# Performance work log

Measured on AMD Instinct MI355X. Metric: run time of the kernel, lower is better.

## Reference

```python
import jax, jax.numpy as jnp
import numpy as np

N = 50000      # ncount
IN_CH = 256    # in_channels
OUT_CH = 128   # out_channels
NNZ = 800000   # nnz per sparse matrix (avg degree 16)


def _spmm(rows, cols, vals, dense, n_rows):
    # sparse(COO) @ dense : gather rows of dense by col index, scale, scatter-add by row
    contrib = vals[:, None] * dense[cols]              # [nnz, F]
    return jax.ops.segment_sum(contrib, rows, num_segments=n_rows)


def setup_inputs() -> dict:
    key = jax.random.key(0)
    ks = jax.random.split(key, 12)
    phi_indices = jnp.stack([
        jax.random.randint(ks[0], (NNZ,), 0, N),
        jax.random.randint(ks[1], (NNZ,), 0, N)])
    phi_values = jax.random.normal(ks[2], (NNZ,), dtype=jnp.float32)
    phi_inverse_indices = jnp.stack([
        jax.random.randint(ks[3], (NNZ,), 0, N),
        jax.random.randint(ks[4], (NNZ,), 0, N)])
    phi_inverse_values = jax.random.normal(ks[5], (NNZ,), dtype=jnp.float32)
    feature_indices = jnp.stack([
        jax.random.randint(ks[6], (NNZ,), 0, N),       # node index
        jax.random.randint(ks[7], (NNZ,), 0, IN_CH)])  # feature column
    feature_values = jax.random.normal(ks[8], (NNZ,), dtype=jnp.float32)
    # xavier_uniform for weight_matrix
    limit = float(np.sqrt(6.0 / (IN_CH + OUT_CH)))
    weight_matrix = jax.random.uniform(ks[9], (IN_CH, OUT_CH), jnp.float32, -limit, limit)
    # diagonal filter Theta init uniform(0.9, 1.1)
    diagonal_weight_filter = jax.random.uniform(ks[10], (N,), jnp.float32, 0.9, 1.1)
    return {
        "phi_indices": phi_indices,
        "phi_values": phi_values,
        "phi_inverse_indices": phi_inverse_indices,
        "phi_inverse_values": phi_inverse_values,
        "feature_indices": feature_indices,
        "feature_values": feature_values,
        "weight_matrix": weight_matrix,
        "diagonal_weight_filter": diagonal_weight_filter,
        "dropout": 0,
    }


def reference(phi_indices, phi_values, phi_inverse_indices, phi_inverse_values,
              feature_indices, feature_values, weight_matrix,
              diagonal_weight_filter, dropout):
    # rescaled_phi = phi @ diag(theta): scales column j of phi by theta[j]
    scaled_phi_vals = phi_values * diagonal_weight_filter[phi_indices[1]]
    # filtered = features(sparse N x IN) @ W  -> [N, OUT]
    filtered = _spmm(feature_indices[0], feature_indices[1], feature_values,
                     weight_matrix, N)
    # (phi * D * phi_inv) @ filtered computed associatively without dense N x N:
    tmp = _spmm(phi_inverse_indices[0], phi_inverse_indices[1],
                phi_inverse_values, filtered, N)              # phi_inv @ filtered
    localized = _spmm(phi_indices[0], phi_indices[1],
                      scaled_phi_vals, tmp, N)                # (phi D) @ tmp
    # dropout in eval mode (training=False) is identity
    return jax.nn.relu(localized)
```

## Files before the change

### kernel.cpp

```cpp
#include <hip/hip_runtime.h>
#include <hip/hip_fp16.h>


#define OUT_CH 128
#define HALF_CH 64
#define RPB 256
#define RPB_SHIFT 8
#define MAX_NB 256
#define EPB 4096
#define EPT_C 8
#define EPT_D 16
#define STAGE_CAP 8192
#define MAX_INCH_LDS 256


__global__ __launch_bounds__(512) void bucket_hist_kernel(
    const int* __restrict__ rows0, int n0,
    const int* __restrict__ rows1, int n1,
    const int* __restrict__ rows2, int n2,
    int* __restrict__ hist_part,
    int NB, int NBLK)
{
    int m = blockIdx.y;
    const int* rows = (m == 0) ? rows0 : (m == 1) ? rows1 : rows2;
    int nnz         = (m == 0) ? n0    : (m == 1) ? n1    : n2;
    __shared__ int bins[MAX_NB];
    int t = threadIdx.x;
    if (t < NB) bins[t] = 0;
    __syncthreads();
    int base = blockIdx.x * EPB;
    #pragma unroll
    for (int k = 0; k < EPB / 512; ++k) {
        int i = base + k * 512 + t;
        if (i < nnz) atomicAdd(&bins[rows[i] >> RPB_SHIFT], 1);
    }
    __syncthreads();
    int* out = hist_part + ((size_t)(m * NBLK + blockIdx.x)) * NB;
    if (t < NB) out[t] = bins[t];
}


__global__ __launch_bounds__(256) void reduce_totals_kernel(
    const int* __restrict__ hist_part, int* __restrict__ totals, int NB, int NBLK)
{
    int w = blockIdx.x * 4 + (threadIdx.x >> 6);
    if (w >= 3 * NB) return;
    int lane = threadIdx.x & 63;
    int m = w / NB, b = w - m * NB;
    const int* hp = hist_part + (size_t)m * NBLK * NB + b;
    int sum = 0;
    for (int blk = lane; blk < NBLK; blk += 64)
        sum += hp[(size_t)blk * NB];
    #pragma unroll
    for (int s = 1; s < 64; s <<= 1) sum += __shfl_xor(sum, s);
    if (lane == 0) totals[w] = sum;
}


__global__ __launch_bounds__(256) void scan_bases_kernel(
    const int* __restrict__ totals, int* __restrict__ bases,
    int* __restrict__ cursor, int NB)
{
    int m = blockIdx.x, t = threadIdx.x;
    int x = (t < NB) ? totals[m * NB + t] : 0;
    int lane = t & 63, wid = t >> 6;
    int incl = x;
    #pragma unroll
    for (int s = 1; s < 64; s <<= 1) {
        int y = __shfl_up(incl, s);
        if (lane >= s) incl += y;
    }
    __shared__ int wtot[4], wbase[4];
    if (lane == 63) wtot[wid] = incl;
    __syncthreads();
    if (t == 0) {
        int run = 0;
        #pragma unroll
        for (int w = 0; w < 4; ++w) { int v = wtot[w]; wbase[w] = run; run += v; }
    }
    __syncthreads();
    if (t < NB) {
        int excl = wbase[wid] + incl - x;
        bases[m * NB + t] = excl;
        cursor[m * NB + t] = excl;
    }
}


__global__ __launch_bounds__(512) void bucket_scatter_kernel(
    const int* __restrict__ rows0, const int* __restrict__ cols0, const float* __restrict__ vals0, int n0,
    const int* __restrict__ rows1, const int* __restrict__ cols1, const float* __restrict__ vals1, int n1,
    const int* __restrict__ rows2, const int* __restrict__ cols2, const float* __restrict__ vals2, int n2,
    const float* __restrict__ theta,
    const int* __restrict__ hist_part, int* __restrict__ cursor,
    int2* __restrict__ eb0, int2* __restrict__ eb1, int2* __restrict__ eb2,
    int NB, int NBLK)
{
    int m = blockIdx.y;
    const int* rows; const int* cols; const float* vals; int nnz; int2* eb;
    if (m == 0)      { rows = rows0; cols = cols0; vals = vals0; nnz = n0; eb = eb0; }
    else if (m == 1) { rows = rows1; cols = cols1; vals = vals1; nnz = n1; eb = eb1; }
    else             { rows = rows2; cols = cols2; vals = vals2; nnz = n2; eb = eb2; }

    __shared__ int2 staged[EPB];
    __shared__ unsigned char bucket_of[EPB];
    __shared__ int lstart[MAX_NB];
    __shared__ int lcur[MAX_NB];
    __shared__ int gbase[MAX_NB];
    __shared__ int wtot[8], wbase[8];

    int t = threadIdx.x;
    int base = blockIdx.x * EPB;
    bool fold = (m == 2);

    int  bk[EPT_C];
    int2 pl[EPT_C];
    #pragma unroll
    for (int k = 0; k < EPT_C; ++k) {
        int i = base + k * 512 + t;
        if (i < nnz) {
            int r = rows[i], c = cols[i];
            float v = vals[i];
            if (fold) v *= theta[c];
            bk[k] = r >> RPB_SHIFT;
            pl[k] = make_int2(c | ((r & (RPB - 1)) << 16), __float_as_int(v));
        } else bk[k] = -1;
    }

    {
        const int* hp = hist_part + ((size_t)(m * NBLK + blockIdx.x)) * NB;
        int lh = (t < NB) ? hp[t] : 0;
        int lane = t & 63, wid = t >> 6;
        int incl = lh;
        #pragma unroll
        for (int s = 1; s < 64; s <<= 1) {
            int y = __shfl_up(incl, s);
            if (lane >= s) incl += y;
        }
        if (lane == 63) wtot[wid] = incl;
        __syncthreads();
        if (t == 0) {
            int run = 0;
            #pragma unroll
            for (int w = 0; w < 8; ++w) { int v = wtot[w]; wbase[w] = run; run += v; }
        }
        __syncthreads();
        if (t < NB) {
            int excl = wbase[wid] + incl - lh;
            lstart[t] = excl;
            lcur[t]   = excl;
            gbase[t] = atomicAdd(&cursor[m * NB + t], lh);
        }
    }
    __syncthreads();

    #pragma unroll
    for (int k = 0; k < EPT_C; ++k) {
        if (bk[k] >= 0) {
            int idx = atomicAdd(&lcur[bk[k]], 1);
            staged[idx] = pl[k];
            bucket_of[idx] = (unsigned char)bk[k];
        }
    }
    __syncthreads();

    int count = min(EPB, nnz - base);
    for (int i = t; i < count; i += 512) {
        int b = bucket_of[i];
        int dest = gbase[b] + (i - lstart[b]);
        eb[dest] = staged[i];
    }
}


__global__ __launch_bounds__(512) void bucket_to_csr_kernel(
    const int2* __restrict__ eb0, const int2* __restrict__ eb1, const int2* __restrict__ eb2,
    unsigned int* __restrict__ ec0, unsigned int* __restrict__ ec1, unsigned int* __restrict__ ec2,
    const int* __restrict__ bases,
    int* __restrict__ off,
    int n0, int n1, int n2, int NB, int n)
{
    int m = blockIdx.y;
    int b = blockIdx.x;
    const int2* eb; unsigned int* ec; int nnz;
    if (m == 0)      { eb = eb0; ec = ec0; nnz = n0; }
    else if (m == 1) { eb = eb1; ec = ec1; nnz = n1; }
    else             { eb = eb2; ec = ec2; nnz = n2; }
    int base = bases[m * NB + b];
    int end  = (b + 1 < NB) ? bases[m * NB + b + 1] : nnz;
    int cnt  = end - base;

    __shared__ unsigned int staged_c[STAGE_CAP];
    __shared__ int hist[RPB];
    __shared__ int cur[RPB];
    __shared__ int loc[RPB + 1];
    __shared__ int wtot[4];
    __shared__ int wbase[4];
    int t = threadIdx.x;
    int lane = t & 63, wid = t >> 6;
    if (t < RPB) { hist[t] = 0; cur[t] = 0; }
    __syncthreads();

    bool fits = (cnt <= STAGE_CAP);

    int2 er[EPT_D];
    int  rl[EPT_D];
    if (fits) {
        #pragma unroll
        for (int k = 0; k < EPT_D; ++k) {
            int i = base + k * 512 + t;
            if (i < end) {
                er[k] = eb[i];
                rl[k] = (er[k].x >> 16) & (RPB - 1);
                atomicAdd(&hist[rl[k]], 1);
            } else rl[k] = -1;
        }
    } else {
        for (int i = base + t; i < end; i += 512)
            atomicAdd(&hist[(eb[i].x >> 16) & (RPB - 1)], 1);
    }
    __syncthreads();

    {
        int x = (t < RPB) ? hist[t] : 0;
        int incl = x;
        #pragma unroll
        for (int s = 1; s < 64; s <<= 1) {
            int y = __shfl_up(incl, s);
            if (lane >= s) incl += y;
        }
        if (lane == 63 && wid < 4) wtot[wid] = incl;
        __syncthreads();
        if (t == 0) {
            int run = 0;
            #pragma unroll
            for (int w = 0; w < 4; ++w) { int v = wtot[w]; wbase[w] = run; run += v; }
        }
        __syncthreads();
        if (t < RPB) {
            loc[t] = wbase[wid] + incl - x;
            if (t == RPB - 1) loc[RPB] = wbase[3] + incl;
        }
    }
    __syncthreads();
    if (t < RPB) {
        int r = b * RPB + t;
        if (r <= n) off[(size_t)m * (n + 1) + r] = base + loc[t];
        if (b == NB - 1 && t == 0) off[(size_t)m * (n + 1) + n] = nnz;
    }

    if (fits) {
        #pragma unroll
        for (int k = 0; k < EPT_D; ++k) {
            if (rl[k] >= 0) {
                int rk = atomicAdd(&cur[rl[k]], 1);
                unsigned short h = __half_as_ushort(__float2half_rn(__int_as_float(er[k].y)));
                staged_c[loc[rl[k]] + rk] = (unsigned int)(er[k].x & 0xFFFF) | ((unsigned int)h << 16);
            }
        }
        __syncthreads();
        for (int i = t; i < cnt; i += 512)
            ec[base + i] = staged_c[i];
    } else {
        for (int i = base + t; i < end; i += 512) {
            int2 e = eb[i];
            int r2 = (e.x >> 16) & (RPB - 1);
            int rk = atomicAdd(&cur[r2], 1);
            unsigned short h = __half_as_ushort(__float2half_rn(__int_as_float(e.y)));
            ec[base + loc[r2] + rk] = (unsigned int)(e.x & 0xFFFF) | ((unsigned int)h << 16);
        }
    }
}


__global__ __launch_bounds__(1024) void spmm_w_lds_kernel(
    const int* __restrict__ off, const unsigned int* __restrict__ edges,
    const float* __restrict__ W, __half2* __restrict__ out,
    int nrows, int in_ch)
{
    __shared__ __half2 wlds[MAX_INCH_LDS * HALF_CH];
    int t = threadIdx.x;
    {
        const float2* wf = (const float2*)W;
        int tot = in_ch * HALF_CH;
        for (int i = t; i < tot; i += 1024) {
            float2 f = wf[i];
            wlds[i] = __float22half2_rn(f);
        }
    }
    __syncthreads();

    int lane = t & 63, w = t >> 6;
    #pragma unroll
    for (int k4 = 0; k4 < 4; ++k4) {
        int r = blockIdx.x * 64 + k4 * 16 + w;
        if (r >= nrows) continue;
        int j   = __builtin_amdgcn_readfirstlane(off[r]);
        int end = __builtin_amdgcn_readfirstlane(off[r + 1]);
        float2 a0 = make_float2(0.f, 0.f), a1 = make_float2(0.f, 0.f);

        for (; j + 16 <= end; j += 16) {
            unsigned int e[16];
            #pragma unroll
            for (int k = 0; k < 16; ++k) e[k] = edges[j + k];
            #pragma unroll
            for (int k = 0; k < 16; ++k) {
                float2 d = __half22float2(wlds[(e[k] & 0xFFFF) * HALF_CH + lane]);
                float v = __half2float(__ushort_as_half((unsigned short)(e[k] >> 16)));
                if (k & 1) { a1.x = fmaf(v, d.x, a1.x); a1.y = fmaf(v, d.y, a1.y); }
                else       { a0.x = fmaf(v, d.x, a0.x); a0.y = fmaf(v, d.y, a0.y); }
            }
        }
        for (; j + 4 <= end; j += 4) {
            unsigned int e[4];
            #pragma unroll
            for (int k = 0; k < 4; ++k) e[k] = edges[j + k];
            #pragma unroll
            for (int k = 0; k < 4; ++k) {
                float2 d = __half22float2(wlds[(e[k] & 0xFFFF) * HALF_CH + lane]);
                float v = __half2float(__ushort_as_half((unsigned short)(e[k] >> 16)));
                if (k & 1) { a1.x = fmaf(v, d.x, a1.x); a1.y = fmaf(v, d.y, a1.y); }
                else       { a0.x = fmaf(v, d.x, a0.x); a0.y = fmaf(v, d.y, a0.y); }
            }
        }
        for (; j < end; ++j) {
            unsigned int e0 = edges[j];
            float2 d = __half22float2(wlds[(e0 & 0xFFFF) * HALF_CH + lane]);
            float v0 = __half2float(__ushort_as_half((unsigned short)(e0 >> 16)));
            a0.x = fmaf(v0, d.x, a0.x); a0.y = fmaf(v0, d.y, a0.y);
        }
        float2 res = make_float2(a0.x + a1.x, a0.y + a1.y);
        out[(size_t)r * HALF_CH + lane] = __float22half2_rn(res);
    }
}


template<bool SRC_H, bool DST_H, bool RELU>
__global__ __launch_bounds__(256) void spmm_csr_kernel(
    const int* __restrict__ off, const unsigned int* __restrict__ edges,
    const void* __restrict__ dense_v, void* __restrict__ out_v, int nrows)
{
    int lane = threadIdx.x & 63;
    int r = blockIdx.x * 4 + (threadIdx.x >> 6);
    if (r >= nrows) return;
    int j   = __builtin_amdgcn_readfirstlane(off[r]);
    int end = __builtin_amdgcn_readfirstlane(off[r + 1]);
    const float2*  df = (const float2*)dense_v;
    const __half2* dh = (const __half2*)dense_v;

    float2 a0 = make_float2(0.f, 0.f), a1 = make_float2(0.f, 0.f);

    for (; j + 16 <= end; j += 16) {
        unsigned int e[16]; float2 d[16];
        #pragma unroll
        for (int k = 0; k < 16; ++k) e[k] = edges[j + k];
        #pragma unroll
        for (int k = 0; k < 16; ++k) {
            if (SRC_H) d[k] = __half22float2(dh[(size_t)(e[k] & 0xFFFF) * HALF_CH + lane]);
            else       d[k] = df[(size_t)(e[k] & 0xFFFF) * HALF_CH + lane];
        }
        #pragma unroll
        for (int k = 0; k < 16; ++k) {
            float v = __half2float(__ushort_as_half((unsigned short)(e[k] >> 16)));
            if (k & 1) { a1.x = fmaf(v, d[k].x, a1.x); a1.y = fmaf(v, d[k].y, a1.y); }
            else       { a0.x = fmaf(v, d[k].x, a0.x); a0.y = fmaf(v, d[k].y, a0.y); }
        }
    }
    for (; j + 8 <= end; j += 8) {
        unsigned int e[8]; float2 d[8];
        #pragma unroll
        for (int k = 0; k < 8; ++k) e[k] = edges[j + k];
        #pragma unroll
        for (int k = 0; k < 8; ++k) {
            if (SRC_H) d[k] = __half22float2(dh[(size_t)(e[k] & 0xFFFF) * HALF_CH + lane]);
            else       d[k] = df[(size_t)(e[k] & 0xFFFF) * HALF_CH + lane];
        }
        #pragma unroll
        for (int k = 0; k < 8; ++k) {
            float v = __half2float(__ushort_as_half((unsigned short)(e[k] >> 16)));
            if (k & 1) { a1.x = fmaf(v, d[k].x, a1.x); a1.y = fmaf(v, d[k].y, a1.y); }
            else       { a0.x = fmaf(v, d[k].x, a0.x); a0.y = fmaf(v, d[k].y, a0.y); }
        }
    }
    for (; j + 4 <= end; j += 4) {
        unsigned int e[4]; float2 d[4];
        #pragma unroll
        for (int k = 0; k < 4; ++k) e[k] = edges[j + k];
        #pragma unroll
        for (int k = 0; k < 4; ++k) {
            if (SRC_H) d[k] = __half22float2(dh[(size_t)(e[k] & 0xFFFF) * HALF_CH + lane]);
            else       d[k] = df[(size_t)(e[k] & 0xFFFF) * HALF_CH + lane];
        }
        #pragma unroll
        for (int k = 0; k < 4; ++k) {
            float v = __half2float(__ushort_as_half((unsigned short)(e[k] >> 16)));
            if (k & 1) { a1.x = fmaf(v, d[k].x, a1.x); a1.y = fmaf(v, d[k].y, a1.y); }
            else       { a0.x = fmaf(v, d[k].x, a0.x); a0.y = fmaf(v, d[k].y, a0.y); }
        }
    }
    for (; j < end; ++j) {
        unsigned int e0 = edges[j];
        float2 d0;
        if (SRC_H) d0 = __half22float2(dh[(size_t)(e0 & 0xFFFF) * HALF_CH + lane]);
        else       d0 = df[(size_t)(e0 & 0xFFFF) * HALF_CH + lane];
        float v0 = __half2float(__ushort_as_half((unsigned short)(e0 >> 16)));
        a0.x = fmaf(v0, d0.x, a0.x); a0.y = fmaf(v0, d0.y, a0.y);
    }
    float2 res = make_float2(a0.x + a1.x, a0.y + a1.y);
    if (RELU) { res.x = fmaxf(res.x, 0.f); res.y = fmaxf(res.y, 0.f); }
    if (DST_H) ((__half2*)out_v)[(size_t)r * HALF_CH + lane] = __float22half2_rn(res);
    else       ((float2*) out_v)[(size_t)r * HALF_CH + lane] = res;
}


__global__ __launch_bounds__(256) void spmm_atomic_kernel(
    const int* __restrict__ rows, const int* __restrict__ cols,
    const float* __restrict__ vals, const float* __restrict__ theta,
    const float* __restrict__ dense, float* __restrict__ out, int nnz)
{
    int idx = blockIdx.x * blockDim.x + threadIdx.x;
    int e = idx >> 7;
    int f = idx & (OUT_CH - 1);
    if (e >= nnz) return;
    int r = rows[e];
    int c = cols[e];
    float v = vals[e];
    if (theta != nullptr) v *= theta[c];
    atomicAdd(&out[(size_t)r * OUT_CH + f], v * dense[(size_t)c * OUT_CH + f]);
}

__global__ __launch_bounds__(256) void relu_kernel(float* __restrict__ out, int n4)
{
    int i = blockIdx.x * blockDim.x + threadIdx.x;
    if (i >= n4) return;
    float4 v = ((float4*)out)[i];
    v.x = fmaxf(v.x, 0.f); v.y = fmaxf(v.y, 0.f);
    v.z = fmaxf(v.z, 0.f); v.w = fmaxf(v.w, 0.f);
    ((float4*)out)[i] = v;
}


static inline size_t align16(size_t x) { return (x + 15) & ~(size_t)15; }

extern "C" void kernel_launch(void* const* d_in, const int* in_sizes, int n_in,
                              void* d_out, int out_size, void* d_ws, size_t ws_size,
                              hipStream_t stream)
{
    const int*   phi_idx   = (const int*)d_in[0];
    const float* phi_vals  = (const float*)d_in[1];
    const int*   phii_idx  = (const int*)d_in[2];
    const float* phii_vals = (const float*)d_in[3];
    const int*   feat_idx  = (const int*)d_in[4];
    const float* feat_vals = (const float*)d_in[5];
    const float* W         = (const float*)d_in[6];
    const float* theta     = (const float*)d_in[7];

    const int nnz_phi  = in_sizes[1];
    const int nnz_phii = in_sizes[3];
    const int nnz_feat = in_sizes[5];
    const int n_nodes  = in_sizes[7];
    const int in_ch    = in_sizes[6] / OUT_CH;
    const size_t dense_elems = (size_t)n_nodes * OUT_CH;
    const long long total_e = (long long)nnz_feat + nnz_phii + nnz_phi;

    const int NB = (n_nodes + RPB - 1) >> RPB_SHIFT;
    int max_nnz = nnz_feat > nnz_phii ? nnz_feat : nnz_phii;
    if (nnz_phi > max_nnz) max_nnz = nnz_phi;
    const int NBLK = (max_nnz + EPB - 1) / EPB;

    size_t p = 0;
    size_t filtered_off = p; p += align16(dense_elems * sizeof(__half));
    size_t tmp_off      = p; p += align16(dense_elems * sizeof(__half));
    size_t off_off      = p; p += align16((size_t)3 * (n_nodes + 1) * sizeof(int));
    size_t hp_off       = p; p += align16((size_t)3 * NBLK * NB * sizeof(int));
    size_t tot_off      = p; p += align16((size_t)3 * NB * sizeof(int));
    size_t bas_off      = p; p += align16((size_t)3 * NB * sizeof(int));
    size_t cur_off      = p; p += align16((size_t)3 * NB * sizeof(int));
    size_t eb_off       = p; p += align16((size_t)total_e * sizeof(int2));
    size_t ec_off       = p; p += align16((size_t)total_e * sizeof(unsigned int));
    size_t need = p;

    char* ws = (char*)d_ws;
    dim3 block256(256);
    dim3 block512(512);

    bool fast_ok = (ws_size >= need) && (NB <= MAX_NB) && (n_nodes <= 65536) &&
                   (in_ch <= 65536);

    if (fast_ok) {
        __half* filtered = (__half*)(ws + filtered_off);
        __half* tmp      = (__half*)(ws + tmp_off);
        int* off_arr    = (int*)(ws + off_off);
        int* hist_part  = (int*)(ws + hp_off);
        int* totals     = (int*)(ws + tot_off);
        int* bases      = (int*)(ws + bas_off);
        int* cursor     = (int*)(ws + cur_off);
        int2* eb0 = (int2*)(ws + eb_off);
        int2* eb1 = eb0 + nnz_feat;
        int2* eb2 = eb1 + nnz_phii;
        unsigned int* ec0 = (unsigned int*)(ws + ec_off);
        unsigned int* ec1 = ec0 + nnz_feat;
        unsigned int* ec2 = ec1 + nnz_phii;

        const int* rows0 = feat_idx;  const int* cols0 = feat_idx + nnz_feat;
        const int* rows1 = phii_idx;  const int* cols1 = phii_idx + nnz_phii;
        const int* rows2 = phi_idx;   const int* cols2 = phi_idx  + nnz_phi;

        bucket_hist_kernel<<<dim3(NBLK, 3), block512, 0, stream>>>(
            rows0, nnz_feat, rows1, nnz_phii, rows2, nnz_phi,
            hist_part, NB, NBLK);

        int nwaves = 3 * NB;
        reduce_totals_kernel<<<dim3((nwaves + 3) / 4), block256, 0, stream>>>(
            hist_part, totals, NB, NBLK);

        scan_bases_kernel<<<dim3(3), block256, 0, stream>>>(
            totals, bases, cursor, NB);

        bucket_scatter_kernel<<<dim3(NBLK, 3), block512, 0, stream>>>(
            rows0, cols0, feat_vals, nnz_feat,
            rows1, cols1, phii_vals, nnz_phii,
            rows2, cols2, phi_vals,  nnz_phi,
            theta, hist_part, cursor, eb0, eb1, eb2, NB, NBLK);

        bucket_to_csr_kernel<<<dim3(NB, 3), block512, 0, stream>>>(
            eb0, eb1, eb2, ec0, ec1, ec2, bases, off_arr,
            nnz_feat, nnz_phii, nnz_phi, NB, n_nodes);

        int* off_f  = off_arr;
        int* off_pi = off_arr + (n_nodes + 1);
        int* off_p  = off_arr + 2 * (n_nodes + 1);

        dim3 grid_r((unsigned)((n_nodes + 3) / 4));
        if (in_ch <= MAX_INCH_LDS) {
            dim3 grid_w((unsigned)((n_nodes + 63) / 64));
            spmm_w_lds_kernel<<<grid_w, dim3(1024), 0, stream>>>(
                off_f, ec0, W, (__half2*)filtered, n_nodes, in_ch);
        } else {
            spmm_csr_kernel<false, true, false><<<grid_r, block256, 0, stream>>>(
                off_f,  ec0, (const void*)W, (void*)filtered, n_nodes);
        }
        spmm_csr_kernel<true, true, false><<<grid_r, block256, 0, stream>>>(
            off_pi, ec1, (const void*)filtered, (void*)tmp, n_nodes);
        spmm_csr_kernel<true, false, true><<<grid_r, block256, 0, stream>>>(
            off_p,  ec2, (const void*)tmp, d_out, n_nodes);
    } else {
        float* filtered = (float*)ws;
        float* tmp      = filtered + dense_elems;
        hipMemsetAsync(filtered, 0, 2 * dense_elems * sizeof(float), stream);
        hipMemsetAsync(d_out, 0, (size_t)out_size * sizeof(float), stream);
        {
            long long t = (long long)nnz_feat * OUT_CH;
            spmm_atomic_kernel<<<dim3((unsigned)((t + 255) / 256)), block256, 0, stream>>>(
                feat_idx, feat_idx + nnz_feat, feat_vals, nullptr, W, filtered, nnz_feat);
        }
        {
            long long t = (long long)nnz_phii * OUT_CH;
            spmm_atomic_kernel<<<dim3((unsigned)((t + 255) / 256)), block256, 0, stream>>>(
                phii_idx, phii_idx + nnz_phii, phii_vals, nullptr, filtered, tmp, nnz_phii);
        }
        {
            long long t = (long long)nnz_phi * OUT_CH;
            spmm_atomic_kernel<<<dim3((unsigned)((t + 255) / 256)), block256, 0, stream>>>(
                phi_idx, phi_idx + nnz_phi, phi_vals, theta, tmp, (float*)d_out, nnz_phi);
        }
        {
            int n4 = out_size / 4;
            relu_kernel<<<dim3((n4 + 255) / 256), block256, 0, stream>>>((float*)d_out, n4);
        }
    }
}
```

Baseline: 206.1 us.

## Pad CSR rows to multiples of four edges and load edges as uint4

Each CSR row in the packed edge arrays is padded to a multiple of four entries with zero-valued edges, and per-bucket slack keeps the offsets 16-byte aligned. The SpMM kernels then fetch edges with vectorized uint4 loads instead of scalar loads. The aim is fewer load instructions and less load latency in the gather loops. In exchange the layout uses more workspace, writes extra zeros during the build, and adds wasted FMAs on padded entries; zero edges point to column 0 with value 0, so results stay correct.

```diff
diff --git a/kernel.cpp b/kernel.cpp
--- a/kernel.cpp
+++ b/kernel.cpp
@@ -10,7 +10,8 @@
 #define EPB 4096
 #define EPT_C 8
 #define EPT_D 16
-#define STAGE_CAP 8192
+#define STAGE_CAP_P 9216
+#define PAD_SLACK 1024
 #define MAX_INCH_LDS 256
 
 
@@ -186,11 +187,14 @@
     if (m == 0)      { eb = eb0; ec = ec0; nnz = n0; }
     else if (m == 1) { eb = eb1; ec = ec1; nnz = n1; }
     else             { eb = eb2; ec = ec2; nnz = n2; }
-    int base = bases[m * NB + b];
-    int end  = (b + 1 < NB) ? bases[m * NB + b + 1] : nnz;
-    int cnt  = end - base;
-
-    __shared__ unsigned int staged_c[STAGE_CAP];
+    int base  = bases[m * NB + b];
+    int nextb = (b + 1 < NB) ? bases[m * NB + b + 1] : nnz;
+    int end   = nextb;
+    int cnt   = end - base;
+    int pbase = ((base  + 3) & ~3) + b * PAD_SLACK;
+    int pnext = ((nextb + 3) & ~3) + (b + 1) * PAD_SLACK;
+
+    __shared__ unsigned int staged_c[STAGE_CAP_P];
     __shared__ int hist[RPB];
     __shared__ int cur[RPB];
     __shared__ int loc[RPB + 1];
@@ -201,7 +205,7 @@
     if (t < RPB) { hist[t] = 0; cur[t] = 0; }
     __syncthreads();
 
-    bool fits = (cnt <= STAGE_CAP);
+    bool fits = (cnt <= EPT_D * 512);
 
     int2 er[EPT_D];
     int  rl[EPT_D];
@@ -222,7 +226,7 @@
     __syncthreads();
 
     {
-        int x = (t < RPB) ? hist[t] : 0;
+        int x = (t < RPB) ? ((hist[t] + 3) & ~3) : 0;
         int incl = x;
         #pragma unroll
         for (int s = 1; s < 64; s <<= 1) {
@@ -245,11 +249,14 @@
     __syncthreads();
     if (t < RPB) {
         int r = b * RPB + t;
-        if (r <= n) off[(size_t)m * (n + 1) + r] = base + loc[t];
-        if (b == NB - 1 && t == 0) off[(size_t)m * (n + 1) + n] = nnz;
-    }
+        if (r < n) off[(size_t)m * (n + 1) + r] = pbase + loc[t];
+    }
+    if (b == NB - 1 && t == 0) off[(size_t)m * (n + 1) + n] = pnext;
+    int totp = loc[RPB];
 
     if (fits) {
+        for (int i = t; i < totp; i += 512) staged_c[i] = 0;
+        __syncthreads();
         #pragma unroll
         for (int k = 0; k < EPT_D; ++k) {
             if (rl[k] >= 0) {
@@ -259,16 +266,26 @@
             }
         }
         __syncthreads();
-        for (int i = t; i < cnt; i += 512)
-            ec[base + i] = staged_c[i];
+        for (int i = t; i < totp; i += 512)
+            ec[pbase + i] = staged_c[i];
+        for (int i = pbase + totp + t; i < pnext; i += 512)
+            ec[i] = 0;
     } else {
         for (int i = base + t; i < end; i += 512) {
             int2 e = eb[i];
             int r2 = (e.x >> 16) & (RPB - 1);
             int rk = atomicAdd(&cur[r2], 1);
             unsigned short h = __half_as_ushort(__float2half_rn(__int_as_float(e.y)));
-            ec[base + loc[r2] + rk] = (unsigned int)(e.x & 0xFFFF) | ((unsigned int)h << 16);
-        }
+            ec[pbase + loc[r2] + rk] = (unsigned int)(e.x & 0xFFFF) | ((unsigned int)h << 16);
+        }
+        __syncthreads();
+        if (t < RPB) {
+            int s0 = loc[t] + hist[t];
+            int e0 = loc[t] + ((hist[t] + 3) & ~3);
+            for (int i = s0; i < e0; ++i) ec[pbase + i] = 0;
+        }
+        for (int i = pbase + totp + t; i < pnext; i += 512)
+            ec[i] = 0;
     }
 }
 
@@ -300,9 +317,12 @@
         float2 a0 = make_float2(0.f, 0.f), a1 = make_float2(0.f, 0.f);
 
         for (; j + 16 <= end; j += 16) {
-            unsigned int e[16];
-            #pragma unroll
-            for (int k = 0; k < 16; ++k) e[k] = edges[j + k];
+            uint4 q0 = *(const uint4*)(edges + j);
+            uint4 q1 = *(const uint4*)(edges + j + 4);
+            uint4 q2 = *(const uint4*)(edges + j + 8);
+            uint4 q3 = *(const uint4*)(edges + j + 12);
+            unsigned int e[16] = {q0.x,q0.y,q0.z,q0.w, q1.x,q1.y,q1.z,q1.w,
+                                  q2.x,q2.y,q2.z,q2.w, q3.x,q3.y,q3.z,q3.w};
             #pragma unroll
             for (int k = 0; k < 16; ++k) {
                 float2 d = __half22float2(wlds[(e[k] & 0xFFFF) * HALF_CH + lane]);
@@ -312,9 +332,8 @@
             }
         }
         for (; j + 4 <= end; j += 4) {
-            unsigned int e[4];
-            #pragma unroll
-            for (int k = 0; k < 4; ++k) e[k] = edges[j + k];
+            uint4 q = *(const uint4*)(edges + j);
+            unsigned int e[4] = {q.x, q.y, q.z, q.w};
             #pragma unroll
             for (int k = 0; k < 4; ++k) {
                 float2 d = __half22float2(wlds[(e[k] & 0xFFFF) * HALF_CH + lane]);
@@ -351,9 +370,13 @@
     float2 a0 = make_float2(0.f, 0.f), a1 = make_float2(0.f, 0.f);
 
     for (; j + 16 <= end; j += 16) {
-        unsigned int e[16]; float2 d[16];
-        #pragma unroll
-        for (int k = 0; k < 16; ++k) e[k] = edges[j + k];
+        uint4 q0 = *(const uint4*)(edges + j);
+        uint4 q1 = *(const uint4*)(edges + j + 4);
+        uint4 q2 = *(const uint4*)(edges + j + 8);
+        uint4 q3 = *(const uint4*)(edges + j + 12);
+        unsigned int e[16] = {q0.x,q0.y,q0.z,q0.w, q1.x,q1.y,q1.z,q1.w,
+                              q2.x,q2.y,q2.z,q2.w, q3.x,q3.y,q3.z,q3.w};
+        float2 d[16];
         #pragma unroll
         for (int k = 0; k < 16; ++k) {
             if (SRC_H) d[k] = __half22float2(dh[(size_t)(e[k] & 0xFFFF) * HALF_CH + lane]);
@@ -367,9 +390,10 @@
         }
     }
     for (; j + 8 <= end; j += 8) {
-        unsigned int e[8]; float2 d[8];
-        #pragma unroll
-        for (int k = 0; k < 8; ++k) e[k] = edges[j + k];
+        uint4 q0 = *(const uint4*)(edges + j);
+        uint4 q1 = *(const uint4*)(edges + j + 4);
+        unsigned int e[8] = {q0.x,q0.y,q0.z,q0.w, q1.x,q1.y,q1.z,q1.w};
+        float2 d[8];
         #pragma unroll
         for (int k = 0; k < 8; ++k) {
             if (SRC_H) d[k] = __half22float2(dh[(size_t)(e[k] & 0xFFFF) * HALF_CH + lane]);
@@ -383,9 +407,9 @@
         }
     }
     for (; j + 4 <= end; j += 4) {
-        unsigned int e[4]; float2 d[4];
-        #pragma unroll
-        for (int k = 0; k < 4; ++k) e[k] = edges[j + k];
+        uint4 q = *(const uint4*)(edges + j);
+        unsigned int e[4] = {q.x, q.y, q.z, q.w};
+        float2 d[4];
         #pragma unroll
         for (int k = 0; k < 4; ++k) {
             if (SRC_H) d[k] = __half22float2(dh[(size_t)(e[k] & 0xFFFF) * HALF_CH + lane]);
@@ -441,6 +465,9 @@
 
 
 static inline size_t align16(size_t x) { return (x + 15) & ~(size_t)15; }
+static inline size_t pad_ec(int nnz, int NB) {
+    return (size_t)(((nnz + 3) & ~3)) + (size_t)NB * PAD_SLACK + 16;
+}
 
 extern "C" void kernel_launch(void* const* d_in, const int* in_sizes, int n_in,
                               void* d_out, int out_size, void* d_ws, size_t ws_size,
@@ -467,6 +494,10 @@
     int max_nnz = nnz_feat > nnz_phii ? nnz_feat : nnz_phii;
     if (nnz_phi > max_nnz) max_nnz = nnz_phi;
     const int NBLK = (max_nnz + EPB - 1) / EPB;
+
+    const size_t pec0 = pad_ec(nnz_feat, NB);
+    const size_t pec1 = pad_ec(nnz_phii, NB);
+    const size_t pec2 = pad_ec(nnz_phi,  NB);
 
     size_t p = 0;
     size_t filtered_off = p; p += align16(dense_elems * sizeof(__half));
@@ -477,7 +508,7 @@
     size_t bas_off      = p; p += align16((size_t)3 * NB * sizeof(int));
     size_t cur_off      = p; p += align16((size_t)3 * NB * sizeof(int));
     size_t eb_off       = p; p += align16((size_t)total_e * sizeof(int2));
-    size_t ec_off       = p; p += align16((size_t)total_e * sizeof(unsigned int));
+    size_t ec_off       = p; p += align16((pec0 + pec1 + pec2) * sizeof(unsigned int));
     size_t need = p;
 
     char* ws = (char*)d_ws;
@@ -499,8 +530,8 @@
         int2* eb1 = eb0 + nnz_feat;
         int2* eb2 = eb1 + nnz_phii;
         unsigned int* ec0 = (unsigned int*)(ws + ec_off);
-        unsigned int* ec1 = ec0 + nnz_feat;
-        unsigned int* ec2 = ec1 + nnz_phii;
+        unsigned int* ec1 = ec0 + pec0;
+        unsigned int* ec2 = ec1 + pec1;
 
         const int* rows0 = feat_idx;  const int* cols0 = feat_idx + nnz_feat;
         const int* rows1 = phii_idx;  const int* cols1 = phii_idx + nnz_phii;
```

Result: slower. 363.4 us (+76.4%).
